# Performance work log

Measured on AMD Instinct MI355X. Metric: run time of the kernel, lower is better.

The kernel has to match this reference:

```python
import jax, jax.numpy as jnp
import numpy as np

L = 2048      # sequence length (self.len)
DIM = 1024    # model dim
DPOS = 128    # positional encoding dim
B = 4
EPS = 1e-5


def make_pe(length, d):
    # standard sinusoidal positional encoding, shape [length, d]
    pos = np.arange(length)[:, None].astype(np.float32)
    div = np.exp(-np.arange(0, d, 2).astype(np.float32) * (np.log(10000.0) / d))
    pe = np.zeros((length, d), dtype=np.float32)
    pe[:, 0::2] = np.sin(pos * div)
    pe[:, 1::2] = np.cos(pos * div)
    return jnp.asarray(pe)


def setup_inputs() -> dict:
    key = jax.random.key(0)
    ks = jax.random.split(key, 16)
    s = lambda fan_in: 1.0 / np.sqrt(fan_in)
    inp = {
        "z": jax.random.normal(ks[0], (B, L, DIM), jnp.float32),
        "x": jax.random.normal(ks[1], (B, L, DIM), jnp.float32),
        "a": jax.random.normal(ks[2], (1,), jnp.float32),
        "pe": make_pe(L, DPOS),
        # torch Linear weights stored [out, in]
        "w_pos1": jax.random.normal(ks[3], (DPOS + DIM, DPOS), jnp.float32) * s(DPOS),
        "b_pos1": jnp.zeros((DPOS + DIM,), jnp.float32),
        "w_pos2": jax.random.normal(ks[4], (DIM, DPOS + DIM), jnp.float32) * s(DPOS + DIM),
        "b_pos2": jnp.zeros((DIM,), jnp.float32),
        "w1": jax.random.normal(ks[5], (DIM * 2, DIM), jnp.float32) * s(DIM),
        "b1": jnp.zeros((DIM * 2,), jnp.float32),
        "w2": jax.random.normal(ks[6], (DIM, DIM * 2), jnp.float32) * s(DIM * 2),
        "b2": jnp.zeros((DIM,), jnp.float32),
        "w3": jax.random.normal(ks[7], (DIM * 2, DIM), jnp.float32) * s(DIM),
        "b3": jnp.zeros((DIM * 2,), jnp.float32),
        "w4": jax.random.normal(ks[8], (DIM, DIM * 2), jnp.float32) * s(DIM * 2),
        "b4": jnp.zeros((DIM,), jnp.float32),
        "ln_g": jnp.ones((DIM,), jnp.float32),
        "ln_b": jnp.zeros((DIM,), jnp.float32),
    }
    return inp


def _layer_norm(v, g, b):
    mu = jnp.mean(v, axis=-1, keepdims=True)
    var = jnp.var(v, axis=-1, keepdims=True)
    return (v - mu) * jax.lax.rsqrt(var + EPS) * g + b


def _lin(v, w, b):
    return v @ w.T + b


def reference(z, x, a, pe, w_pos1, b_pos1, w_pos2, b_pos2,
              w1, b1, w2, b2, w3, b3, w4, b4, ln_g, ln_b):
    zn = _layer_norm(z, ln_g, ln_b)                       # [B, L, D]
    fz = jnp.fft.rfft(zn, n=2 * L, axis=1)                # [B, L+1, D] complex
    expa = jnp.exp(a)                                     # [1]
    window = jnp.exp(-jnp.arange(L, dtype=jnp.float32) * expa)  # [L]
    h = _lin(pe, w_pos1, b_pos1)                          # [L, DPOS+D]
    h = jax.nn.gelu(h, approximate=False)
    h = _lin(h, w_pos2, b_pos2)                           # [L, D] (dropout eval = id)
    wfh = jnp.fft.rfft(window[:, None] * h, n=2 * L, axis=0)  # [L+1, D]
    cwhz = jnp.fft.irfft(wfh * fz, axis=1)[:, :L, :]      # [B, L, D]
    x1 = _lin(x, w1, b1)
    x1 = jax.nn.gelu(x1, approximate=False)
    x1 = _lin(x1, w2, b2)
    x1 = x1 * cwhz + z
    y = _layer_norm(x1, ln_g, ln_b)
    y = _lin(y, w3, b3)
    y = jax.nn.gelu(y, approximate=False)
    y = _lin(y, w4, b4)
    return y + x1
```

## Files before the change

### kernel.cpp

```cpp
#include <hip/hip_runtime.h>
#include <hip/hip_bf16.h>
#include <cmath>

typedef __hip_bfloat16 bf16;
typedef __attribute__((ext_vector_type(8))) short bf16x8;
typedef __attribute__((ext_vector_type(4))) float f32x4;

static __device__ __forceinline__ float b2f(bf16 v) { return __bfloat162float(v); }
static __device__ __forceinline__ bf16 f2b(float v) { return __float2bfloat16(v); }

static __device__ __forceinline__ void gl2lds16(const bf16* g, bf16* l) {
  __builtin_amdgcn_global_load_lds(
      (const __attribute__((address_space(1))) void*)g,
      (__attribute__((address_space(3))) void*)l, 16, 0, 0);
}

static __device__ __forceinline__ float gelu_fast(float v) {
  float u = v * (0.7978845608f + 0.0356774081f * v * v);
  float e = __expf(2.f * u);
  return v * (e * __frcp_rn(e + 1.f));
}

struct CvtSegs { const float* src[7]; int blk_off[8]; };
__global__ __launch_bounds__(256) void cvt7_k(CvtSegs s, bf16* __restrict__ dst0)
{
  int b = blockIdx.x;
  int seg = 0;
#pragma unroll
  for (int i = 0; i < 6; ++i) seg += (b >= s.blk_off[i + 1]) ? 1 : 0;
  const float* src = s.src[seg] + (size_t)(b - s.blk_off[seg]) * 1024;
  bf16* dst = dst0 + (size_t)b * 1024;
  int idx = threadIdx.x * 4;
  float4 v = *(const float4*)(src + idx);
  union { bf16 bb[4]; ushort4 u; } o;
  o.bb[0] = f2b(v.x); o.bb[1] = f2b(v.y); o.bb[2] = f2b(v.z); o.bb[3] = f2b(v.w);
  *(ushort4*)(dst + idx) = o.u;
}

__global__ __launch_bounds__(256) void cvt_k(const float* __restrict__ in,
                                             bf16* __restrict__ out, int n)
{
  int idx = (blockIdx.x * 256 + threadIdx.x) * 4;
  if (idx >= n) return;
  float4 v = *(const float4*)(in + idx);
  union { bf16 b[4]; ushort4 u; } o;
  o.b[0] = f2b(v.x); o.b[1] = f2b(v.y); o.b[2] = f2b(v.z); o.b[3] = f2b(v.w);
  *(ushort4*)(out + idx) = o.u;
}

__global__ __launch_bounds__(256) void ln_k(const float* __restrict__ X, bf16* __restrict__ Y,
                                            const float* __restrict__ gamma,
                                            const float* __restrict__ beta)
{
  __shared__ float red[16];
  const int row = blockIdx.x, tid = threadIdx.x;
  const float* xr = X + (size_t)row * 1024;
  float v[4], s = 0.f, s2 = 0.f;
#pragma unroll
  for (int i = 0; i < 4; ++i) {
    float xv = xr[tid + i * 256];
    v[i] = xv; s += xv; s2 += xv * xv;
  }
#pragma unroll
  for (int m = 32; m; m >>= 1) { s += __shfl_xor(s, m, 64); s2 += __shfl_xor(s2, m, 64); }
  const int wid = tid >> 6;
  if ((tid & 63) == 0) { red[wid] = s; red[wid + 8] = s2; }
  __syncthreads();
  s  = red[0] + red[1] + red[2] + red[3];
  s2 = red[8] + red[9] + red[10] + red[11];
  const float mu  = s * (1.f / 1024.f);
  const float var = s2 * (1.f / 1024.f) - mu * mu;
  const float rs  = rsqrtf(var + 1e-5f);
#pragma unroll
  for (int i = 0; i < 4; ++i) {
    int c = tid + i * 256;
    Y[(size_t)row * 1024 + c] = f2b((v[i] - mu) * rs * gamma[c] + beta[c]);
  }
}

template<int EPI>
__global__ __launch_bounds__(256, 3) void gemm_k(
    const bf16* __restrict__ A, const bf16* __restrict__ W,
    const float* __restrict__ bias, void* __restrict__ Out,
    const void* __restrict__ aux0, const void* __restrict__ aux1,
    int M, int N, int K)
{
  __shared__ bf16 As[3][128 * 32];
  __shared__ bf16 Bs[3][128 * 32];
  const int tid = threadIdx.x;
  const int wid = tid >> 6, lane = tid & 63;
  const int quad = lane >> 4, l16 = lane & 15;
  const int wm = wid >> 1, wn = wid & 1;
  const int m0 = blockIdx.y * 128, n0 = blockIdx.x * 128;

  f32x4 acc[4][4];
#pragma unroll
  for (int i = 0; i < 4; ++i)
#pragma unroll
    for (int j = 0; j < 4; ++j) acc[i][j] = (f32x4){0.f, 0.f, 0.f, 0.f};

  const bf16 *ga[2], *gb[2];
  int ldso[2];
#pragma unroll
  for (int r = 0; r < 2; ++r) {
    int p = r * 256 + wid * 64 + lane;
    int row = p >> 2;
    int sko = ((p & 3) ^ ((p >> 3) & 3)) << 3;
    ga[r] = A + (size_t)(m0 + row) * K + sko;
    gb[r] = W + (size_t)(n0 + row) * K + sko;
    ldso[r] = (r * 256 + wid * 64) * 8;
  }
  int apos[4], bpos[4];
#pragma unroll
  for (int i = 0; i < 4; ++i) {
    int ar = wm * 64 + i * 16 + l16;
    apos[i] = (ar * 4 + (quad ^ ((ar >> 1) & 3))) * 8;
    int br = wn * 64 + i * 16 + l16;
    bpos[i] = (br * 4 + (quad ^ ((br >> 1) & 3))) * 8;
  }

  const int niter = K >> 5;

#pragma unroll
  for (int t = 0; t < 2; ++t) {
#pragma unroll
    for (int r = 0; r < 2; ++r) {
      gl2lds16(ga[r] + t * 32, &As[t][ldso[r]]);
      gl2lds16(gb[r] + t * 32, &Bs[t][ldso[r]]);
    }
  }

  int cur = 0;
  for (int k = 0; k < niter; ++k) {
    if (k == niter - 1) { asm volatile("s_waitcnt vmcnt(0)" ::: "memory"); }
    else               { asm volatile("s_waitcnt vmcnt(4)" ::: "memory"); }
    asm volatile("s_barrier" ::: "memory");

    const bf16* as = As[cur];
    const bf16* bs = Bs[cur];
    bf16x8 af[4], bfr[4];
#pragma unroll
    for (int i = 0; i < 4; ++i) af[i]  = *(const bf16x8*)(as + apos[i]);
#pragma unroll
    for (int j = 0; j < 4; ++j) bfr[j] = *(const bf16x8*)(bs + bpos[j]);
    asm volatile("s_waitcnt lgkmcnt(0)" ::: "memory");

    if (k + 2 < niter) {
      int nb = cur + 2; if (nb >= 3) nb -= 3;
#pragma unroll
      for (int r = 0; r < 2; ++r) {
        gl2lds16(ga[r] + (k + 2) * 32, &As[nb][ldso[r]]);
        gl2lds16(gb[r] + (k + 2) * 32, &Bs[nb][ldso[r]]);
      }
    }

#pragma unroll
    for (int i = 0; i < 4; ++i)
#pragma unroll
      for (int j = 0; j < 4; ++j)
        acc[i][j] = __builtin_amdgcn_mfma_f32_16x16x32_bf16(af[i], bfr[j], acc[i][j], 0, 0, 0);

    cur += 1; if (cur == 3) cur = 0;
  }

  float expa = 0.f;
  if (EPI == 1) expa = expf(((const float*)aux0)[0]);

#pragma unroll
  for (int i = 0; i < 4; ++i) {
    const int gm_base = m0 + wm * 64 + i * 16 + quad * 4;
#pragma unroll
    for (int j = 0; j < 4; ++j) {
      const int gn = n0 + wn * 64 + j * 16 + l16;
      const float bv = bias[gn];
#pragma unroll
      for (int r = 0; r < 4; ++r) {
        const int gm = gm_base + r;
        const size_t off = (size_t)gm * N + gn;
        float v = acc[i][j][r] + bv;
        if (EPI == 0) {
          ((bf16*)Out)[off] = f2b(gelu_fast(v));
        } else if (EPI == 1) {
          ((float*)Out)[off] = v * expf(-(float)gm * expa);
        } else if (EPI == 2) {
          ((float*)Out)[off] = v * ((const float*)aux0)[off] + ((const float*)aux1)[off];
        } else {
          ((float*)Out)[off] = v + ((const float*)aux0)[off];
        }
      }
    }
  }
}

__global__ __launch_bounds__(256) void conv_k(
    const bf16* __restrict__ zn,
    const float* __restrict__ wh,
    const float* __restrict__ a,
    float* __restrict__ out)
{
  __shared__ float whs[64 * 64];
  __shared__ float znt[128 * 64];
  const int tid = threadIdx.x;
  const int dd = tid & 63, ttg = tid >> 6;
  const int t0 = blockIdx.x * 64, d0 = blockIdx.y * 64, b = blockIdx.z;
  const float expa = expf(a[0]);
  const float smax = 20.7f / expa;

  float acc[16];
#pragma unroll
  for (int q = 0; q < 16; ++q) acc[q] = 0.f;

  for (int sb = 0; sb <= t0 + 63; sb += 64) {
    if ((float)sb > smax) break;
    for (int idx = tid; idx < 64 * 64; idx += 256) {
      int ss = idx >> 6, d2 = idx & 63;
      int s = sb + ss;
      whs[idx] = (s < 2048) ? wh[(size_t)s * 1024 + d0 + d2] : 0.f;
    }
    for (int idx = tid; idx < 128 * 64; idx += 256) {
      int r = idx >> 6, d2 = idx & 63;
      int u = t0 - sb - 64 + r;
      znt[idx] = (u >= 0) ? b2f(zn[((size_t)b * 2048 + u) * 1024 + d0 + d2]) : 0.f;
    }
    __syncthreads();

    float win[16];
#pragma unroll
    for (int q = 0; q < 16; ++q) win[q] = znt[(ttg * 16 + q + 64) * 64 + dd];

#pragma unroll
    for (int ss = 0; ss < 64; ++ss) {
      float wv = whs[ss * 64 + dd];
#pragma unroll
      for (int q = 0; q < 16; ++q) acc[q] += wv * win[q];
      if (ss < 63) {
#pragma unroll
        for (int q = 15; q >= 1; --q) win[q] = win[q - 1];
        win[0] = znt[(ttg * 16 + 63 - ss) * 64 + dd];
      }
    }
    __syncthreads();
  }
#pragma unroll
  for (int q = 0; q < 16; ++q) {
    int t = t0 + ttg * 16 + q;
    out[((size_t)b * 2048 + t) * 1024 + d0 + dd] = acc[q];
  }
}

extern "C" void kernel_launch(void* const* d_in, const int* in_sizes, int n_in,
                              void* d_out, int out_size, void* d_ws, size_t ws_size,
                              hipStream_t stream)
{
  const float* z      = (const float*)d_in[0];
  const float* x      = (const float*)d_in[1];
  const float* a      = (const float*)d_in[2];
  const float* pe     = (const float*)d_in[3];
  const float* w_pos1 = (const float*)d_in[4];
  const float* b_pos1 = (const float*)d_in[5];
  const float* w_pos2 = (const float*)d_in[6];
  const float* b_pos2 = (const float*)d_in[7];
  const float* w1     = (const float*)d_in[8];
  const float* b1     = (const float*)d_in[9];
  const float* w2     = (const float*)d_in[10];
  const float* b2     = (const float*)d_in[11];
  const float* w3     = (const float*)d_in[12];
  const float* b3     = (const float*)d_in[13];
  const float* w4     = (const float*)d_in[14];
  const float* b4     = (const float*)d_in[15];
  const float* ln_g   = (const float*)d_in[16];
  const float* ln_b   = (const float*)d_in[17];

  char* ws = (char*)d_ws;
  bf16* pe_bf  = (bf16*)(ws + 0);
  bf16* wp1_bf = (bf16*)(ws + 524288);
  bf16* wp2_bf = (bf16*)(ws + 819200);
  bf16* w1_bf  = (bf16*)(ws + 3178496);
  bf16* w2_bf  = (bf16*)(ws + 7372800);
  bf16* w3_bf  = (bf16*)(ws + 11567104);
  bf16* w4_bf  = (bf16*)(ws + 15761408);
  bf16* h1     = (bf16*)(ws + 19955712);
  bf16* zn_bf  = (bf16*)(ws + 24674304);
  bf16* x_bf   = (bf16*)(ws + 41451520);
  float* wh    = (float*)(ws + 58228736);
  float* cwhz  = (float*)(ws + 66617344);
  bf16*  x1n   = (bf16*)(ws + 66617344);
  bf16*  g     = (bf16*)(ws + 100171776);
  float* x1    = (float*)(ws + 24674304);
  float* out   = (float*)d_out;

  CvtSegs segs;
  segs.src[0] = pe;  segs.src[1] = w_pos1; segs.src[2] = w_pos2;
  segs.src[3] = w1;  segs.src[4] = w2;     segs.src[5] = w3; segs.src[6] = w4;
  int bo[8] = {0, 256, 400, 1552, 3600, 5648, 7696, 9744};
  for (int i = 0; i < 8; ++i) segs.blk_off[i] = bo[i];
  cvt7_k<<<9744, 256, 0, stream>>>(segs, (bf16*)ws);
  cvt_k<<<8192, 256, 0, stream>>>(x, x_bf, 8388608);

  ln_k<<<8192, 256, 0, stream>>>(z, zn_bf, ln_g, ln_b);
  gemm_k<0><<<dim3(9, 16), 256, 0, stream>>>(pe_bf, wp1_bf, b_pos1, h1, nullptr, nullptr, 2048, 1152, 128);
  gemm_k<1><<<dim3(8, 16), 256, 0, stream>>>(h1, wp2_bf, b_pos2, wh, a, nullptr, 2048, 1024, 1152);
  conv_k<<<dim3(32, 16, 4), 256, 0, stream>>>(zn_bf, wh, a, cwhz);
  gemm_k<0><<<dim3(16, 64), 256, 0, stream>>>(x_bf, w1_bf, b1, g, nullptr, nullptr, 8192, 2048, 1024);
  gemm_k<2><<<dim3(8, 64), 256, 0, stream>>>(g, w2_bf, b2, x1, cwhz, z, 8192, 1024, 2048);
  ln_k<<<8192, 256, 0, stream>>>(x1, x1n, ln_g, ln_b);
  gemm_k<0><<<dim3(16, 64), 256, 0, stream>>>(x1n, w3_bf, b3, g, nullptr, nullptr, 8192, 2048, 1024);
  gemm_k<3><<<dim3(8, 64), 256, 0, stream>>>(g, w4_bf, b4, out, x1, nullptr, 8192, 1024, 2048);
}
```

Measured before the change: 479.7 us.

## Use 128x256 GEMM tiles for big MLP GEMMs, vectorize layernorm and conv loads

New measurement: 444.9 us. 1.08x faster.

```diff
diff --git a/kernel.cpp b/kernel.cpp
--- a/kernel.cpp
+++ b/kernel.cpp
@@ -8,6 +8,9 @@
 
 static __device__ __forceinline__ float b2f(bf16 v) { return __bfloat162float(v); }
 static __device__ __forceinline__ bf16 f2b(float v) { return __float2bfloat16(v); }
+static __device__ __forceinline__ float us2f(unsigned short u) {
+  return __uint_as_float(((unsigned)u) << 16);
+}
 
 static __device__ __forceinline__ void gl2lds16(const bf16* g, bf16* l) {
   __builtin_amdgcn_global_load_lds(
@@ -54,13 +57,9 @@
 {
   __shared__ float red[16];
   const int row = blockIdx.x, tid = threadIdx.x;
-  const float* xr = X + (size_t)row * 1024;
-  float v[4], s = 0.f, s2 = 0.f;
-#pragma unroll
-  for (int i = 0; i < 4; ++i) {
-    float xv = xr[tid + i * 256];
-    v[i] = xv; s += xv; s2 += xv * xv;
-  }
+  float4 v = *(const float4*)(X + (size_t)row * 1024 + tid * 4);
+  float s  = v.x + v.y + v.z + v.w;
+  float s2 = v.x * v.x + v.y * v.y + v.z * v.z + v.w * v.w;
 #pragma unroll
   for (int m = 32; m; m >>= 1) { s += __shfl_xor(s, m, 64); s2 += __shfl_xor(s2, m, 64); }
   const int wid = tid >> 6;
@@ -71,11 +70,14 @@
   const float mu  = s * (1.f / 1024.f);
   const float var = s2 * (1.f / 1024.f) - mu * mu;
   const float rs  = rsqrtf(var + 1e-5f);
-#pragma unroll
-  for (int i = 0; i < 4; ++i) {
-    int c = tid + i * 256;
-    Y[(size_t)row * 1024 + c] = f2b((v[i] - mu) * rs * gamma[c] + beta[c]);
-  }
+  float4 g = *(const float4*)(gamma + tid * 4);
+  float4 bt = *(const float4*)(beta + tid * 4);
+  union { bf16 b[4]; ushort4 u; } o;
+  o.b[0] = f2b((v.x - mu) * rs * g.x + bt.x);
+  o.b[1] = f2b((v.y - mu) * rs * g.y + bt.y);
+  o.b[2] = f2b((v.z - mu) * rs * g.z + bt.z);
+  o.b[3] = f2b((v.w - mu) * rs * g.w + bt.w);
+  *(ushort4*)(Y + (size_t)row * 1024 + tid * 4) = o.u;
 }
 
 template<int EPI>
@@ -120,15 +122,13 @@
   }
 
   const int niter = K >> 5;
-
-#pragma unroll
-  for (int t = 0; t < 2; ++t) {
+#pragma unroll
+  for (int t = 0; t < 2; ++t)
 #pragma unroll
     for (int r = 0; r < 2; ++r) {
       gl2lds16(ga[r] + t * 32, &As[t][ldso[r]]);
       gl2lds16(gb[r] + t * 32, &Bs[t][ldso[r]]);
     }
-  }
 
   int cur = 0;
   for (int k = 0; k < niter; ++k) {
@@ -153,19 +153,16 @@
         gl2lds16(gb[r] + (k + 2) * 32, &Bs[nb][ldso[r]]);
       }
     }
-
 #pragma unroll
     for (int i = 0; i < 4; ++i)
 #pragma unroll
       for (int j = 0; j < 4; ++j)
         acc[i][j] = __builtin_amdgcn_mfma_f32_16x16x32_bf16(af[i], bfr[j], acc[i][j], 0, 0, 0);
-
     cur += 1; if (cur == 3) cur = 0;
   }
 
   float expa = 0.f;
   if (EPI == 1) expa = expf(((const float*)aux0)[0]);
-
 #pragma unroll
   for (int i = 0; i < 4; ++i) {
     const int gm_base = m0 + wm * 64 + i * 16 + quad * 4;
@@ -178,15 +175,120 @@
         const int gm = gm_base + r;
         const size_t off = (size_t)gm * N + gn;
         float v = acc[i][j][r] + bv;
-        if (EPI == 0) {
-          ((bf16*)Out)[off] = f2b(gelu_fast(v));
-        } else if (EPI == 1) {
-          ((float*)Out)[off] = v * expf(-(float)gm * expa);
-        } else if (EPI == 2) {
-          ((float*)Out)[off] = v * ((const float*)aux0)[off] + ((const float*)aux1)[off];
-        } else {
-          ((float*)Out)[off] = v + ((const float*)aux0)[off];
-        }
+        if (EPI == 0) ((bf16*)Out)[off] = f2b(gelu_fast(v));
+        else if (EPI == 1) ((float*)Out)[off] = v * expf(-(float)gm * expa);
+        else if (EPI == 2) ((float*)Out)[off] = v * ((const float*)aux0)[off] + ((const float*)aux1)[off];
+        else ((float*)Out)[off] = v + ((const float*)aux0)[off];
+      }
+    }
+  }
+}
+
+template<int EPI>
+__global__ __launch_bounds__(256, 2) void gemm256_k(
+    const bf16* __restrict__ A, const bf16* __restrict__ W,
+    const float* __restrict__ bias, void* __restrict__ Out,
+    const void* __restrict__ aux0, const void* __restrict__ aux1,
+    int M, int N, int K)
+{
+  __shared__ bf16 As[3][128 * 32];
+  __shared__ bf16 Bs[3][256 * 32];
+  const int tid = threadIdx.x;
+  const int wid = tid >> 6, lane = tid & 63;
+  const int quad = lane >> 4, l16 = lane & 15;
+  const int wm = wid >> 1, wn = wid & 1;
+  const int m0 = blockIdx.y * 128, n0 = blockIdx.x * 256;
+
+  f32x4 acc[4][8];
+#pragma unroll
+  for (int i = 0; i < 4; ++i)
+#pragma unroll
+    for (int j = 0; j < 8; ++j) acc[i][j] = (f32x4){0.f, 0.f, 0.f, 0.f};
+
+  const bf16 *ga[2], *gb[4];
+  int ldsoA[2], ldsoB[4];
+#pragma unroll
+  for (int r = 0; r < 2; ++r) {
+    int p = r * 256 + tid;
+    int row = p >> 2;
+    int sko = ((p & 3) ^ ((p >> 3) & 3)) << 3;
+    ga[r] = A + (size_t)(m0 + row) * K + sko;
+    ldsoA[r] = (r * 256 + wid * 64) * 8;
+  }
+#pragma unroll
+  for (int r = 0; r < 4; ++r) {
+    int p = r * 256 + tid;
+    int row = p >> 2;
+    int sko = ((p & 3) ^ ((p >> 3) & 3)) << 3;
+    gb[r] = W + (size_t)(n0 + row) * K + sko;
+    ldsoB[r] = (r * 256 + wid * 64) * 8;
+  }
+  int apos[4], bpos[8];
+#pragma unroll
+  for (int i = 0; i < 4; ++i) {
+    int ar = wm * 64 + i * 16 + l16;
+    apos[i] = (ar * 4 + (quad ^ ((ar >> 1) & 3))) * 8;
+  }
+#pragma unroll
+  for (int j = 0; j < 8; ++j) {
+    int br = wn * 128 + j * 16 + l16;
+    bpos[j] = (br * 4 + (quad ^ ((br >> 1) & 3))) * 8;
+  }
+
+  const int niter = K >> 5;
+#pragma unroll
+  for (int t = 0; t < 2; ++t) {
+#pragma unroll
+    for (int r = 0; r < 2; ++r) gl2lds16(ga[r] + t * 32, &As[t][ldsoA[r]]);
+#pragma unroll
+    for (int r = 0; r < 4; ++r) gl2lds16(gb[r] + t * 32, &Bs[t][ldsoB[r]]);
+  }
+
+  int cur = 0;
+  for (int k = 0; k < niter; ++k) {
+    if (k == niter - 1) { asm volatile("s_waitcnt vmcnt(0)" ::: "memory"); }
+    else               { asm volatile("s_waitcnt vmcnt(6)" ::: "memory"); }
+    asm volatile("s_barrier" ::: "memory");
+
+    const bf16* as = As[cur];
+    const bf16* bs = Bs[cur];
+    bf16x8 af[4], bfr[8];
+#pragma unroll
+    for (int i = 0; i < 4; ++i) af[i]  = *(const bf16x8*)(as + apos[i]);
+#pragma unroll
+    for (int j = 0; j < 8; ++j) bfr[j] = *(const bf16x8*)(bs + bpos[j]);
+    asm volatile("s_waitcnt lgkmcnt(0)" ::: "memory");
+
+    if (k + 2 < niter) {
+      int nb = cur + 2; if (nb >= 3) nb -= 3;
+#pragma unroll
+      for (int r = 0; r < 2; ++r) gl2lds16(ga[r] + (k + 2) * 32, &As[nb][ldsoA[r]]);
+#pragma unroll
+      for (int r = 0; r < 4; ++r) gl2lds16(gb[r] + (k + 2) * 32, &Bs[nb][ldsoB[r]]);
+    }
+#pragma unroll
+    for (int i = 0; i < 4; ++i)
+#pragma unroll
+      for (int j = 0; j < 8; ++j)
+        acc[i][j] = __builtin_amdgcn_mfma_f32_16x16x32_bf16(af[i], bfr[j], acc[i][j], 0, 0, 0);
+    cur += 1; if (cur == 3) cur = 0;
+  }
+
+#pragma unroll
+  for (int i = 0; i < 4; ++i) {
+    const int gm_base = m0 + wm * 64 + i * 16 + quad * 4;
+#pragma unroll
+    for (int j = 0; j < 8; ++j) {
+      const int gn = n0 + wn * 128 + j * 16 + l16;
+      const float bv = bias[gn];
+#pragma unroll
+      for (int r = 0; r < 4; ++r) {
+        const int gm = gm_base + r;
+        const size_t off = (size_t)gm * N + gn;
+        float v = acc[i][j][r] + bv;
+        if (EPI == 0) ((bf16*)Out)[off] = f2b(gelu_fast(v));
+        else if (EPI == 2) ((float*)Out)[off] = v * ((const float*)aux0)[off] + ((const float*)aux1)[off];
+        else ((float*)Out)[off] = v + ((const float*)aux0)[off];
       }
     }
   }
@@ -205,6 +307,7 @@
   const int t0 = blockIdx.x * 64, d0 = blockIdx.y * 64, b = blockIdx.z;
   const float expa = expf(a[0]);
   const float smax = 20.7f / expa;
+  const unsigned short* znu = (const unsigned short*)zn;
 
   float acc[16];
 #pragma unroll
@@ -212,22 +315,39 @@
 
   for (int sb = 0; sb <= t0 + 63; sb += 64) {
     if ((float)sb > smax) break;
-    for (int idx = tid; idx < 64 * 64; idx += 256) {
-      int ss = idx >> 6, d2 = idx & 63;
-      int s = sb + ss;
-      whs[idx] = (s < 2048) ? wh[(size_t)s * 1024 + d0 + d2] : 0.f;
-    }
-    for (int idx = tid; idx < 128 * 64; idx += 256) {
-      int r = idx >> 6, d2 = idx & 63;
-      int u = t0 - sb - 64 + r;
-      znt[idx] = (u >= 0) ? b2f(zn[((size_t)b * 2048 + u) * 1024 + d0 + d2]) : 0.f;
+    float4 wv4[4];
+#pragma unroll
+    for (int i = 0; i < 4; ++i) {
+      int cc = tid + 256 * i;
+      int row = cc >> 4, dq = (cc & 15) * 4;
+      wv4[i] = *(const float4*)&wh[(size_t)(sb + row) * 1024 + d0 + dq];
+    }
+    ushort4 zv4[8];
+#pragma unroll
+    for (int i = 0; i < 8; ++i) {
+      int cc = tid + 256 * i;
+      int row = cc >> 4, dq = (cc & 15) * 4;
+      int u = t0 - sb - 64 + row;
+      zv4[i] = (u >= 0) ? *(const ushort4*)&znu[((size_t)b * 2048 + u) * 1024 + d0 + dq]
+                        : make_ushort4(0, 0, 0, 0);
+    }
+#pragma unroll
+    for (int i = 0; i < 4; ++i) {
+      int cc = tid + 256 * i;
+      *(float4*)&whs[(cc >> 4) * 64 + (cc & 15) * 4] = wv4[i];
+    }
+#pragma unroll
+    for (int i = 0; i < 8; ++i) {
+      int cc = tid + 256 * i;
+      float4 o;
+      o.x = us2f(zv4[i].x); o.y = us2f(zv4[i].y); o.z = us2f(zv4[i].z); o.w = us2f(zv4[i].w);
+      *(float4*)&znt[(cc >> 4) * 64 + (cc & 15) * 4] = o;
     }
     __syncthreads();
 
     float win[16];
 #pragma unroll
     for (int q = 0; q < 16; ++q) win[q] = znt[(ttg * 16 + q + 64) * 64 + dd];
-
 #pragma unroll
     for (int ss = 0; ss < 64; ++ss) {
       float wv = whs[ss * 64 + dd];
@@ -301,9 +421,9 @@
   gemm_k<0><<<dim3(9, 16), 256, 0, stream>>>(pe_bf, wp1_bf, b_pos1, h1, nullptr, nullptr, 2048, 1152, 128);
   gemm_k<1><<<dim3(8, 16), 256, 0, stream>>>(h1, wp2_bf, b_pos2, wh, a, nullptr, 2048, 1024, 1152);
   conv_k<<<dim3(32, 16, 4), 256, 0, stream>>>(zn_bf, wh, a, cwhz);
-  gemm_k<0><<<dim3(16, 64), 256, 0, stream>>>(x_bf, w1_bf, b1, g, nullptr, nullptr, 8192, 2048, 1024);
-  gemm_k<2><<<dim3(8, 64), 256, 0, stream>>>(g, w2_bf, b2, x1, cwhz, z, 8192, 1024, 2048);
+  gemm256_k<0><<<dim3(8, 64), 256, 0, stream>>>(x_bf, w1_bf, b1, g, nullptr, nullptr, 8192, 2048, 1024);
+  gemm256_k<2><<<dim3(4, 64), 256, 0, stream>>>(g, w2_bf, b2, x1, cwhz, z, 8192, 1024, 2048);
   ln_k<<<8192, 256, 0, stream>>>(x1, x1n, ln_g, ln_b);
-  gemm_k<0><<<dim3(16, 64), 256, 0, stream>>>(x1n, w3_bf, b3, g, nullptr, nullptr, 8192, 2048, 1024);
-  gemm_k<3><<<dim3(8, 64), 256, 0, stream>>>(g, w4_bf, b4, out, x1, nullptr, 8192, 1024, 2048);
-}
+  gemm256_k<0><<<dim3(8, 64), 256, 0, stream>>>(x1n, w3_bf, b3, g, nullptr, nullptr, 8192, 2048, 1024);
+  gemm256_k<3><<<dim3(4, 64), 256, 0, stream>>>(g, w4_bf, b4, out, x1, nullptr, 8192, 1024, 2048);
+}
```
